# Optimization experiments

Measured on AMD Instinct MI355X. Metric: run time of the kernel, lower is better.

The kernel has to match this reference:

```python
import jax, jax.numpy as jnp
import numpy as np

NUM_LAYERS = 2
MAG = 5 / 10.0  # magnitude=5 on a 0-10 scale
FILL = 0.5      # gray fill for out-of-bounds pixels (images in [0,1])
ENH = 1.0 + 0.9 * MAG  # enhancement factor magnitude (brightness/contrast/sharpness)


def _bilinear(img, xi, yi):
    H, W, _ = img.shape
    x0 = jnp.floor(xi); y0 = jnp.floor(yi)
    wx = xi - x0; wy = yi - y0
    def gather(yy, xx):
        valid = (xx >= 0) & (xx <= W - 1) & (yy >= 0) & (yy <= H - 1)
        v = img[jnp.clip(yy, 0, H - 1).astype(jnp.int32),
                jnp.clip(xx, 0, W - 1).astype(jnp.int32)]
        return jnp.where(valid[..., None], v, FILL)
    return (gather(y0, x0) * ((1 - wx) * (1 - wy))[..., None]
            + gather(y0, x0 + 1) * (wx * (1 - wy))[..., None]
            + gather(y0 + 1, x0) * ((1 - wx) * wy)[..., None]
            + gather(y0 + 1, x0 + 1) * (wx * wy)[..., None])


def _affine(img, a, b, tx, c, d, ty):
    # inverse affine map about image center, bilinear resample
    H, W, _ = img.shape
    ys, xs = jnp.meshgrid(jnp.arange(H, dtype=jnp.float32),
                          jnp.arange(W, dtype=jnp.float32), indexing='ij')
    cx = (W - 1) * 0.5; cy = (H - 1) * 0.5
    xi = a * (xs - cx) + b * (ys - cy) + tx + cx
    yi = c * (xs - cx) + d * (ys - cy) + ty + cy
    return _bilinear(img, xi, yi)


def _blend(a, b, f):
    return jnp.clip(a + f * (b - a), 0.0, 1.0)


def _smooth(img):
    # 3x3 smoothing kernel used by PIL/TF sharpness
    k = jnp.array([[1., 1., 1.], [1., 5., 1.], [1., 1., 1.]], jnp.float32) / 13.0
    H, W, _ = img.shape
    p = jnp.pad(img, ((1, 1), (1, 1), (0, 0)), mode='edge')
    out = jnp.zeros_like(img)
    for i in range(3):
        for j in range(3):
            out = out + k[i, j] * p[i:i + H, j:j + W]
    return out


def _rotate(img, s):
    th = s * (30.0 * MAG) * (np.pi / 180.0)
    co, si = jnp.cos(th), jnp.sin(th)
    return _affine(img, co, si, 0.0, -si, co, 0.0)

def _shear_x(img, s):
    sh = s * 0.3 * MAG
    return _affine(img, 1.0, -sh, 0.0, 0.0, 1.0, 0.0)

def _shear_y(img, s):
    sh = s * 0.3 * MAG
    return _affine(img, 1.0, 0.0, 0.0, -sh, 1.0, 0.0)

def _trans_x(img, s):
    t = s * 0.3 * MAG * img.shape[1]
    return _affine(img, 1.0, 0.0, -t, 0.0, 1.0, 0.0)

def _trans_y(img, s):
    t = s * 0.3 * MAG * img.shape[0]
    return _affine(img, 1.0, 0.0, 0.0, 0.0, 1.0, -t)

def _brightness(img, s):
    f = jnp.where(s > 0, ENH, 1.0 / ENH)
    return _blend(jnp.zeros_like(img), img, f)

def _contrast(img, s):
    f = jnp.where(s > 0, ENH, 1.0 / ENH)
    return _blend(jnp.mean(img) * jnp.ones_like(img), img, f)

def _sharpness(img, s):
    f = jnp.where(s > 0, ENH, 1.0 / ENH)
    return _blend(_smooth(img), img, f)


BRANCHES = [_rotate, _shear_x, _shear_y, _trans_x, _trans_y,
            _brightness, _contrast, _sharpness]


def _apply_one(img, ops, signs):
    # img: [H,W,3]; ops, signs: [NUM_LAYERS]
    for l in range(NUM_LAYERS):
        s = (2 * signs[l] - 1).astype(jnp.float32)
        img = jax.lax.switch(ops[l], BRANCHES, img, s)
    return img


def setup_inputs() -> dict:
    key = jax.random.key(0)
    k1, k2, k3 = jax.random.split(key, 3)
    B, H, W = 64, 512, 512
    images = jax.random.uniform(k1, (B, H, W, 3), dtype=jnp.float32)
    op_ids = jax.random.randint(k2, (B, NUM_LAYERS), 0, len(BRANCHES), dtype=jnp.int32)
    signs = jax.random.randint(k3, (B, NUM_LAYERS), 0, 2, dtype=jnp.int32)
    return {"images": images, "op_ids": op_ids, "signs": signs}


def reference(images, op_ids, signs):
    return jax.vmap(_apply_one)(images, op_ids, signs)
```

## Files before the change

kernel.cpp:

```cpp
#include <hip/hip_runtime.h>
#include <math.h>

#define IMH 512
#define IMW 512
#define NIMG 64
#define NPIX (IMH*IMW)
#define NELEM (NPIX*3)
#define CXF 255.5f
#define CYF 255.5f
#define ENHF 1.45f
#define INVENHF (1.0f/1.45f)
#define FILLF 0.5f
#define MBPI0 64
#define MBPI1 512
#define TW 32
#define TH 32
#define MAXLDS 1800

struct F3 { float x, y, z; };

__device__ __forceinline__ F3 mk3(float v){ F3 r; r.x=v; r.y=v; r.z=v; return r; }

__device__ __forceinline__ F3 ldpix(const float* __restrict__ im, int y, int x){
  const float* p = im + (y*IMW + x)*3;
  F3 r; r.x=p[0]; r.y=p[1]; r.z=p[2]; return r;
}

__device__ __forceinline__ F3 clip01(F3 v){
  F3 r;
  r.x = fminf(fmaxf(v.x, 0.f), 1.f);
  r.y = fminf(fmaxf(v.y, 0.f), 1.f);
  r.z = fminf(fmaxf(v.z, 0.f), 1.f);
  return r;
}

__device__ __forceinline__ void affine_params(int op, float s,
    float& a, float& b, float& tx, float& c, float& d, float& ty){
  a = 1.f; b = 0.f; tx = 0.f; c = 0.f; d = 1.f; ty = 0.f;
  if (op == 0){
    a = 0.96592582628907f; b = s * 0.25881904510252f; c = -b; d = a;
  } else if (op == 1){
    b = -s * 0.15f;
  } else if (op == 2){
    c = -s * 0.15f;
  } else if (op == 3){
    tx = -s * 76.8f;
  } else if (op == 4){
    ty = -s * 76.8f;
  }
}

__device__ __forceinline__ F3 bilin_img(const float* __restrict__ im, float xi, float yi){
  float x0f = floorf(xi), y0f = floorf(yi);
  float wx = xi - x0f, wy = yi - y0f;
  float w00 = (1.f-wx)*(1.f-wy), w01 = wx*(1.f-wy);
  float w10 = (1.f-wx)*wy,       w11 = wx*wy;
  int x0 = (int)x0f, y0 = (int)y0f;
  F3 r;
  if (x0 >= 0 && y0 >= 0 && x0 < IMW-1 && y0 < IMH-1){
    const float* p0 = im + (y0*IMW + x0)*3;
    const float* p1 = p0 + IMW*3;
    r.x = w00*p0[0] + w01*p0[3] + w10*p1[0] + w11*p1[3];
    r.y = w00*p0[1] + w01*p0[4] + w10*p1[1] + w11*p1[4];
    r.z = w00*p0[2] + w01*p0[5] + w10*p1[2] + w11*p1[5];
  } else {
    r = mk3(0.f);
    #pragma unroll
    for (int cidx = 0; cidx < 4; cidx++){
      int dx = cidx & 1, dy = cidx >> 1;
      int xx = x0 + dx, yy = y0 + dy;
      float w = (dx ? wx : (1.f - wx)) * (dy ? wy : (1.f - wy));
      F3 v;
      if (xx >= 0 && xx < IMW && yy >= 0 && yy < IMH)
        v = ldpix(im, yy, xx);
      else
        v = mk3(FILLF);
      r.x += w * v.x; r.y += w * v.y; r.z += w * v.z;
    }
  }
  return r;
}

__device__ F3 eval0(const float* __restrict__ im, int op, float s, float mean0, int x, int y){
  if (op < 5){
    float a,b,tx,c,d,ty; affine_params(op, s, a, b, tx, c, d, ty);
    float fx = (float)x - CXF, fy = (float)y - CYF;
    return bilin_img(im, a*fx + b*fy + tx + CXF, c*fx + d*fy + ty + CYF);
  }
  F3 v = ldpix(im, y, x);
  float f = (s > 0.f) ? ENHF : INVENHF;
  if (op == 5){
    F3 r; r.x = f*v.x; r.y = f*v.y; r.z = f*v.z; return clip01(r);
  }
  if (op == 6){
    F3 r;
    r.x = mean0 + f*(v.x - mean0);
    r.y = mean0 + f*(v.y - mean0);
    r.z = mean0 + f*(v.z - mean0);
    return clip01(r);
  }
  F3 sm; sm.x = (5.f/13.f)*v.x; sm.y = (5.f/13.f)*v.y; sm.z = (5.f/13.f)*v.z;
  #pragma unroll
  for (int dy = -1; dy <= 1; dy++){
    #pragma unroll
    for (int dx = -1; dx <= 1; dx++){
      if (dx == 0 && dy == 0) continue;
      int yy = min(max(y + dy, 0), IMH-1);
      int xx = min(max(x + dx, 0), IMW-1);
      F3 q = ldpix(im, yy, xx);
      sm.x += (1.f/13.f)*q.x; sm.y += (1.f/13.f)*q.y; sm.z += (1.f/13.f)*q.z;
    }
  }
  F3 r;
  r.x = sm.x + f*(v.x - sm.x);
  r.y = sm.y + f*(v.y - sm.y);
  r.z = sm.z + f*(v.z - sm.z);
  return clip01(r);
}

__device__ __forceinline__ float block_reduce(float v){
  #pragma unroll
  for (int off = 32; off > 0; off >>= 1) v += __shfl_down(v, off, 64);
  __shared__ float sm[4];
  int lane = threadIdx.x & 63, wid = threadIdx.x >> 6;
  if (lane == 0) sm[wid] = v;
  __syncthreads();
  float r = 0.f;
  if (threadIdx.x == 0) r = sm[0] + sm[1] + sm[2] + sm[3];
  return r;
}

__global__ __launch_bounds__(256) void mean0_kernel(const float* __restrict__ images,
    const int* __restrict__ ops, float* __restrict__ means){
  int img = blockIdx.x / MBPI0;
  if (ops[2*img] != 6) return;
  const float4* im = (const float4*)(images + (size_t)img * NELEM);
  float s = 0.f;
  for (int i = (blockIdx.x % MBPI0)*256 + threadIdx.x; i < NELEM/4; i += MBPI0*256){
    float4 v = im[i];
    s += v.x + v.y + v.z + v.w;
  }
  s = block_reduce(s);
  if (threadIdx.x == 0) atomicAdd(&means[2*img], s * (1.0f/(float)NELEM));
}

__global__ __launch_bounds__(256) void mean1_kernel(const float* __restrict__ images,
    const int* __restrict__ ops, const int* __restrict__ signs, float* __restrict__ means){
  int img = blockIdx.x / MBPI1;
  if (ops[2*img + 1] != 6) return;
  int op0 = ops[2*img];
  float s0 = signs[2*img] ? 1.f : -1.f;
  float mean0 = means[2*img];
  const float* im = images + (size_t)img * NELEM;
  float s = 0.f;
  for (int p = (blockIdx.x % MBPI1)*256 + threadIdx.x; p < NPIX; p += MBPI1*256){
    F3 v = eval0(im, op0, s0, mean0, p & (IMW-1), p >> 9);
    s += v.x + v.y + v.z;
  }
  s = block_reduce(s);
  if (threadIdx.x == 0) atomicAdd(&means[2*img + 1], s * (1.0f/(float)NELEM));
}

__device__ __forceinline__ void store4(float* __restrict__ out, int img, int y, int xbase,
                                       const F3* res){
  float4 o0 = make_float4(res[0].x, res[0].y, res[0].z, res[1].x);
  float4 o1 = make_float4(res[1].y, res[1].z, res[2].x, res[2].y);
  float4 o2 = make_float4(res[2].z, res[3].x, res[3].y, res[3].z);
  float4* op = (float4*)(out + ((size_t)img * NPIX + (size_t)y * IMW + xbase) * 3);
  op[0] = o0; op[1] = o1; op[2] = o2;
}

__global__ __launch_bounds__(256) void apply_kernel(const float* __restrict__ images,
    const int* __restrict__ ops, const int* __restrict__ signs,
    const float* __restrict__ means, float* __restrict__ out){
  int img  = blockIdx.x >> 8;
  int tile = blockIdx.x & 255;
  int tx0 = (tile & 15) * TW;
  int ty0 = (tile >> 4) * TH;
  const float* im = images + (size_t)img * NELEM;
  int op0 = ops[2*img], op1 = ops[2*img + 1];
  float s0 = signs[2*img]     ? 1.f : -1.f;
  float s1 = signs[2*img + 1] ? 1.f : -1.f;
  float mean0 = means[2*img], mean1 = means[2*img + 1];

  int row   = threadIdx.x >> 3;
  int xbase = tx0 + ((threadIdx.x & 7) << 2);
  int y     = ty0 + row;
  float f1 = (s1 > 0.f) ? ENHF : INVENHF;

  if (op1 == 5 || op1 == 6){
    F3 res[4];
    #pragma unroll
    for (int q = 0; q < 4; q++){
      F3 v = eval0(im, op0, s0, mean0, xbase + q, y);
      F3 o;
      if (op1 == 5){
        o.x = f1*v.x; o.y = f1*v.y; o.z = f1*v.z;
      } else {
        o.x = mean1 + f1*(v.x - mean1);
        o.y = mean1 + f1*(v.y - mean1);
        o.z = mean1 + f1*(v.z - mean1);
      }
      res[q] = clip01(o);
    }
    store4(out, img, y, xbase, res);
    return;
  }

  float a1=1.f,b1=0.f,txx=0.f,c1=0.f,d1=1.f,tyy=0.f;
  int bx0, by0, bx1, by1;
  if (op1 < 5){
    affine_params(op1, s1, a1, b1, txx, c1, d1, tyy);
    float xmin = 1e30f, xmax = -1e30f, ymin = 1e30f, ymax = -1e30f;
    #pragma unroll
    for (int i = 0; i < 4; i++){
      float fx = (float)(tx0 + (i & 1) * (TW - 1)) - CXF;
      float fy = (float)(ty0 + (i >> 1) * (TH - 1)) - CYF;
      float xi = a1*fx + b1*fy + txx + CXF;
      float yi = c1*fx + d1*fy + tyy + CYF;
      xmin = fminf(xmin, xi); xmax = fmaxf(xmax, xi);
      ymin = fminf(ymin, yi); ymax = fmaxf(ymax, yi);
    }
    bx0 = (int)floorf(xmin) - 1; bx1 = (int)floorf(xmax) + 2;
    by0 = (int)floorf(ymin) - 1; by1 = (int)floorf(ymax) + 2;
  } else {
    bx0 = tx0 - 1; bx1 = tx0 + TW; by0 = ty0 - 1; by1 = ty0 + TH;
  }
  bx0 = max(bx0, 0); by0 = max(by0, 0);
  bx1 = min(bx1, IMW - 1); by1 = min(by1, IMH - 1);
  int bw = bx1 - bx0 + 1, bh = by1 - by0 + 1;
  int nstage = (bw > 0 && bh > 0) ? bw * bh : 0;

  __shared__ float lds[MAXLDS * 3];
  for (int idx = threadIdx.x; idx < nstage; idx += 256){
    int iy = idx / bw;
    int ix = idx - iy * bw;
    F3 v = eval0(im, op0, s0, mean0, bx0 + ix, by0 + iy);
    lds[idx*3 + 0] = v.x; lds[idx*3 + 1] = v.y; lds[idx*3 + 2] = v.z;
  }
  __syncthreads();

  F3 res[4];
  #pragma unroll
  for (int q = 0; q < 4; q++){
    int x = xbase + q;
    F3 o;
    if (op1 < 5){
      float fx = (float)x - CXF, fy = (float)y - CYF;
      float xi = a1*fx + b1*fy + txx + CXF;
      float yi = c1*fx + d1*fy + tyy + CYF;
      float xf0 = floorf(xi), yf0 = floorf(yi);
      float wx = xi - xf0, wy = yi - yf0;
      float w00 = (1.f-wx)*(1.f-wy), w01 = wx*(1.f-wy);
      float w10 = (1.f-wx)*wy,       w11 = wx*wy;
      int x0 = (int)xf0, y0 = (int)yf0;
      if (x0 >= 0 && y0 >= 0 && x0 < IMW-1 && y0 < IMH-1){
        const float* q0 = lds + ((y0 - by0) * bw + (x0 - bx0)) * 3;
        const float* q1 = q0 + bw * 3;
        o.x = w00*q0[0] + w01*q0[3] + w10*q1[0] + w11*q1[3];
        o.y = w00*q0[1] + w01*q0[4] + w10*q1[1] + w11*q1[4];
        o.z = w00*q0[2] + w01*q0[5] + w10*q1[2] + w11*q1[5];
      } else {
        o = mk3(0.f);
        #pragma unroll
        for (int ci = 0; ci < 4; ci++){
          int dx = ci & 1, dy = ci >> 1;
          int xx = x0 + dx, yy = y0 + dy;
          float w = (dx ? wx : (1.f - wx)) * (dy ? wy : (1.f - wy));
          F3 v;
          if (xx >= 0 && xx < IMW && yy >= 0 && yy < IMH){
            int li = ((yy - by0) * bw + (xx - bx0)) * 3;
            v.x = lds[li]; v.y = lds[li+1]; v.z = lds[li+2];
          } else v = mk3(FILLF);
          o.x += w * v.x; o.y += w * v.y; o.z += w * v.z;
        }
      }
    } else {
      int li0 = ((y - by0) * bw + (x - bx0)) * 3;
      F3 v; v.x = lds[li0]; v.y = lds[li0+1]; v.z = lds[li0+2];
      F3 sm; sm.x = (5.f/13.f)*v.x; sm.y = (5.f/13.f)*v.y; sm.z = (5.f/13.f)*v.z;
      #pragma unroll
      for (int dy = -1; dy <= 1; dy++){
        #pragma unroll
        for (int dx = -1; dx <= 1; dx++){
          if (dx == 0 && dy == 0) continue;
          int yy = min(max(y + dy, 0), IMH-1);
          int xx = min(max(x + dx, 0), IMW-1);
          int li = ((yy - by0) * bw + (xx - bx0)) * 3;
          sm.x += (1.f/13.f)*lds[li];
          sm.y += (1.f/13.f)*lds[li+1];
          sm.z += (1.f/13.f)*lds[li+2];
        }
      }
      o.x = sm.x + f1*(v.x - sm.x);
      o.y = sm.y + f1*(v.y - sm.y);
      o.z = sm.z + f1*(v.z - sm.z);
    }
    res[q] = clip01(o);
  }

  store4(out, img, y, xbase, res);
}

extern "C" void kernel_launch(void* const* d_in, const int* in_sizes, int n_in,
                              void* d_out, int out_size, void* d_ws, size_t ws_size,
                              hipStream_t stream){
  const float* images = (const float*)d_in[0];
  const int*   ops    = (const int*)d_in[1];
  const int*   signs  = (const int*)d_in[2];
  float* out   = (float*)d_out;
  float* means = (float*)d_ws;

  hipMemsetAsync(means, 0, 2*NIMG*sizeof(float), stream);
  mean0_kernel<<<NIMG*MBPI0, 256, 0, stream>>>(images, ops, means);
  mean1_kernel<<<NIMG*MBPI1, 256, 0, stream>>>(images, ops, signs, means);
  apply_kernel<<<NIMG*256, 256, 0, stream>>>(images, ops, signs, means, out);
}
```

Before: 424.8 us.

## Fuse layer-1 contrast mean into apply kernel with in-place fixup pass

Drops the separate mean1 pass, which recomputed the layer-0 result just to get the layer-1 contrast mean. The apply kernel now writes the unclipped layer-0 result for contrast images and accumulates the mean with a block reduction and an atomic add. A new fixup kernel then rereads those images' output and applies the contrast blend and clip in place. This trades a full recompute of eval0 for an extra read and write of the output, but only for images whose second op is contrast.

```diff
diff --git a/kernel.cpp b/kernel.cpp
--- a/kernel.cpp
+++ b/kernel.cpp
@@ -12,7 +12,6 @@
 #define INVENHF (1.0f/1.45f)
 #define FILLF 0.5f
 #define MBPI0 64
-#define MBPI1 512
 #define TW 32
 #define TH 32
 #define MAXLDS 1800
@@ -144,23 +143,6 @@
   if (threadIdx.x == 0) atomicAdd(&means[2*img], s * (1.0f/(float)NELEM));
 }
 
-__global__ __launch_bounds__(256) void mean1_kernel(const float* __restrict__ images,
-    const int* __restrict__ ops, const int* __restrict__ signs, float* __restrict__ means){
-  int img = blockIdx.x / MBPI1;
-  if (ops[2*img + 1] != 6) return;
-  int op0 = ops[2*img];
-  float s0 = signs[2*img] ? 1.f : -1.f;
-  float mean0 = means[2*img];
-  const float* im = images + (size_t)img * NELEM;
-  float s = 0.f;
-  for (int p = (blockIdx.x % MBPI1)*256 + threadIdx.x; p < NPIX; p += MBPI1*256){
-    F3 v = eval0(im, op0, s0, mean0, p & (IMW-1), p >> 9);
-    s += v.x + v.y + v.z;
-  }
-  s = block_reduce(s);
-  if (threadIdx.x == 0) atomicAdd(&means[2*img + 1], s * (1.0f/(float)NELEM));
-}
-
 __device__ __forceinline__ void store4(float* __restrict__ out, int img, int y, int xbase,
                                        const F3* res){
   float4 o0 = make_float4(res[0].x, res[0].y, res[0].z, res[1].x);
@@ -172,7 +154,7 @@
 
 __global__ __launch_bounds__(256) void apply_kernel(const float* __restrict__ images,
     const int* __restrict__ ops, const int* __restrict__ signs,
-    const float* __restrict__ means, float* __restrict__ out){
+    float* __restrict__ means, float* __restrict__ out){
   int img  = blockIdx.x >> 8;
   int tile = blockIdx.x & 255;
   int tx0 = (tile & 15) * TW;
@@ -181,7 +163,7 @@
   int op0 = ops[2*img], op1 = ops[2*img + 1];
   float s0 = signs[2*img]     ? 1.f : -1.f;
   float s1 = signs[2*img + 1] ? 1.f : -1.f;
-  float mean0 = means[2*img], mean1 = means[2*img + 1];
+  float mean0 = means[2*img];
 
   int row   = threadIdx.x >> 3;
   int xbase = tx0 + ((threadIdx.x & 7) << 2);
@@ -190,20 +172,23 @@
 
   if (op1 == 5 || op1 == 6){
     F3 res[4];
+    float ssum = 0.f;
     #pragma unroll
     for (int q = 0; q < 4; q++){
       F3 v = eval0(im, op0, s0, mean0, xbase + q, y);
-      F3 o;
       if (op1 == 5){
-        o.x = f1*v.x; o.y = f1*v.y; o.z = f1*v.z;
+        F3 o; o.x = f1*v.x; o.y = f1*v.y; o.z = f1*v.z;
+        res[q] = clip01(o);
       } else {
-        o.x = mean1 + f1*(v.x - mean1);
-        o.y = mean1 + f1*(v.y - mean1);
-        o.z = mean1 + f1*(v.z - mean1);
+        res[q] = v;
+        ssum += v.x + v.y + v.z;
       }
-      res[q] = clip01(o);
     }
     store4(out, img, y, xbase, res);
+    if (op1 == 6){
+      ssum = block_reduce(ssum);
+      if (threadIdx.x == 0) atomicAdd(&means[2*img + 1], ssum * (1.0f/(float)NELEM));
+    }
     return;
   }
 
@@ -302,6 +287,25 @@
   store4(out, img, y, xbase, res);
 }
 
+__global__ __launch_bounds__(256) void fixup_kernel(const int* __restrict__ ops,
+    const int* __restrict__ signs, const float* __restrict__ means,
+    float* __restrict__ out){
+  int img = blockIdx.x >> 8;
+  if (ops[2*img + 1] != 6) return;
+  float f = signs[2*img + 1] ? ENHF : INVENHF;
+  float m = means[2*img + 1];
+  float4* p = (float4*)(out + (size_t)img * NELEM);
+  const int n = NELEM / 4;
+  for (int i = (blockIdx.x & 255)*256 + threadIdx.x; i < n; i += 256*256){
+    float4 v = p[i];
+    v.x = fminf(fmaxf(m + f*(v.x - m), 0.f), 1.f);
+    v.y = fminf(fmaxf(m + f*(v.y - m), 0.f), 1.f);
+    v.z = fminf(fmaxf(m + f*(v.z - m), 0.f), 1.f);
+    v.w = fminf(fmaxf(m + f*(v.w - m), 0.f), 1.f);
+    p[i] = v;
+  }
+}
+
 extern "C" void kernel_launch(void* const* d_in, const int* in_sizes, int n_in,
                               void* d_out, int out_size, void* d_ws, size_t ws_size,
                               hipStream_t stream){
@@ -313,6 +317,6 @@
 
   hipMemsetAsync(means, 0, 2*NIMG*sizeof(float), stream);
   mean0_kernel<<<NIMG*MBPI0, 256, 0, stream>>>(images, ops, means);
-  mean1_kernel<<<NIMG*MBPI1, 256, 0, stream>>>(images, ops, signs, means);
   apply_kernel<<<NIMG*256, 256, 0, stream>>>(images, ops, signs, means, out);
-}
+  fixup_kernel<<<NIMG*256, 256, 0, stream>>>(ops, signs, means, out);
+}
```

Measured after the change: 409.4 us. 3.6% less time.
